# Kernel optimization log

Hardware: AMD Instinct MI355X
Metric: run time of the kernel (lower is better)

## Reference

```python
import jax, jax.numpy as jnp
import numpy as np

B, S, D = 32, 1024, 1024
A = 256           # adapter_size
E = 16            # num_domains
LN_EPS = 1e-5


def setup_inputs() -> dict:
    key = jax.random.key(0)
    ks = jax.random.split(key, 10)
    s = lambda fan_in: 1.0 / np.sqrt(fan_in)
    return {
        'hidden_states': jax.random.normal(ks[0], (B, S, D), dtype=jnp.float32),
        'domain_id': jax.random.randint(ks[1], (B,), 0, E, dtype=jnp.int64),
        'down_W': jax.random.uniform(ks[2], (A, D), jnp.float32, -s(D), s(D)),
        'down_b': jax.random.uniform(ks[3], (A,), jnp.float32, -s(D), s(D)),
        'up_W': jax.random.uniform(ks[4], (D, A), jnp.float32, -s(A), s(A)),
        'up_b': jax.random.uniform(ks[5], (D,), jnp.float32, -s(A), s(A)),
        'expert_W': jax.random.uniform(ks[6], (E, A, A), jnp.float32, -s(A), s(A)),
        'expert_b': jax.random.uniform(ks[7], (E, A), jnp.float32, -s(A), s(A)),
        'domain_emb': jax.random.normal(ks[8], (E, A), dtype=jnp.float32),
        'ln_gamma': jnp.ones((D,), jnp.float32),
        'ln_beta': jnp.zeros((D,), jnp.float32),
    }


def reference(hidden_states, domain_id, down_W, down_b, up_W, up_b,
              expert_W, expert_b, domain_emb, ln_gamma, ln_beta):
    residual = hidden_states
    # down projection + exact GELU (torch nn.GELU default)
    hidden = jnp.einsum('bsd,ad->bsa', hidden_states, down_W) + down_b
    hidden = jax.nn.gelu(hidden, approximate=False)
    # per-sample expert linear: gather each sample's expert weight, batched GEMM
    valid = (domain_id >= 0) & (domain_id < E)
    idx = jnp.clip(domain_id, 0, E - 1)
    Wsel = expert_W[idx]                      # [B, A, A]
    bsel = expert_b[idx]                      # [B, A]
    expert_out = jnp.einsum('bsa,boa->bso', hidden, Wsel) + bsel[:, None, :]
    domain_output = jnp.where(valid[:, None, None], expert_out, hidden)
    # add domain embedding broadcast over seq
    hidden = domain_output + domain_emb[idx][:, None, :]
    # up projection (dropout is identity at inference)
    hidden = jnp.einsum('bsa,da->bsd', hidden, up_W) + up_b
    # layer norm over last dim
    x = hidden + residual
    mu = jnp.mean(x, axis=-1, keepdims=True)
    var = jnp.mean(jnp.square(x - mu), axis=-1, keepdims=True)
    return (x - mu) * jax.lax.rsqrt(var + LN_EPS) * ln_gamma + ln_beta
```

## Files before the change

kernel.cpp:

```cpp
#include <hip/hip_runtime.h>
#include <hip/hip_bf16.h>
#include <math.h>

#define D_DIM 1024
#define A_DIM 256
#define E_NUM 16

typedef __attribute__((ext_vector_type(8))) short short8;
typedef __attribute__((ext_vector_type(4))) float f32x4;

__device__ __forceinline__ short f2bs(float x) {
    __hip_bfloat16 h = __float2bfloat16(x);
    return __builtin_bit_cast(short, h);
}
__device__ __forceinline__ float bs2f(short s) {
    __hip_bfloat16 h = __builtin_bit_cast(__hip_bfloat16, s);
    return __bfloat162float(h);
}
__device__ __forceinline__ float gelu_exact(float x) {
    return 0.5f * x * (1.0f + erff(x * 0.70710678118654752f));
}
__device__ __forceinline__ void gload_lds16(const void* g, void* l) {
    __builtin_amdgcn_global_load_lds(
        (const __attribute__((address_space(1))) void*)g,
        (__attribute__((address_space(3))) void*)l, 16, 0, 0);
}
__device__ __forceinline__ short8 pack8(float4 u, float4 v) {
    short8 pk;
    pk[0] = f2bs(u.x); pk[1] = f2bs(u.y); pk[2] = f2bs(u.z); pk[3] = f2bs(u.w);
    pk[4] = f2bs(v.x); pk[5] = f2bs(v.y); pk[6] = f2bs(v.z); pk[7] = f2bs(v.w);
    return pk;
}

__global__ __launch_bounds__(256) void k_cast_w(
    const float* __restrict__ Wd, const float* __restrict__ Wu,
    const float* __restrict__ eW,
    short* __restrict__ WdB, short* __restrict__ WuB, short* __restrict__ eWB)
{
    unsigned i = blockIdx.x * 256 + threadIdx.x;
    if (i < 131072) {
        const float4* s = (const float4*)eW;
        ((short8*)eWB)[i] = pack8(s[2 * (size_t)i], s[2 * (size_t)i + 1]);
    } else if (i < 163840) {
        unsigned j = i - 131072;
        const float4* s = (const float4*)Wd;
        ((short8*)WdB)[j] = pack8(s[2 * (size_t)j], s[2 * (size_t)j + 1]);
    } else {
        unsigned j = i - 163840;
        const float4* s = (const float4*)Wu;
        ((short8*)WuB)[j] = pack8(s[2 * (size_t)j], s[2 * (size_t)j + 1]);
    }
}

__global__ __launch_bounds__(256, 2) void k_down_expert(
    const float* __restrict__ X, const short* __restrict__ WdB,
    const float* __restrict__ bd, const short* __restrict__ eWB,
    const float* __restrict__ eb, const float* __restrict__ emb,
    const int* __restrict__ domain_id, short* __restrict__ H2)
{
    __shared__ short As[64][72];
    __shared__ short Bs[256][64];
    __shared__ short Hs[64][264];
    const int tid  = threadIdx.x;
    const int lane = tid & 63;
    const int w    = tid >> 6;
    const int quad = lane >> 4, cid = lane & 15;
    const int m0 = blockIdx.x * 64;

    const int samp = m0 >> 10;
    const int id = domain_id[samp];
    const bool valid = (id >= 0) && (id < E_NUM);
    const int idc = id < 0 ? 0 : (id > E_NUM - 1 ? E_NUM - 1 : id);

    f32x4 acc[4][4];
    #pragma unroll
    for (int i = 0; i < 4; i++)
        #pragma unroll
        for (int j = 0; j < 4; j++) acc[i][j] = (f32x4)(0.f);

    for (int kt = 0; kt < D_DIM; kt += 64) {
        #pragma unroll
        for (int p = 0; p < 8; p++) {
            int jj = tid + p * 256;
            int r = jj >> 3;
            int cg = (((jj & 7) ^ (r & 7)) * 8);
            int cl = (jj & 7) * 8;
            gload_lds16(WdB + (size_t)r * D_DIM + kt + cg, &Bs[r][cl]);
        }
        #pragma unroll
        for (int p = 0; p < 2; p++) {
            int jj = tid + p * 256;
            int r = jj >> 3, c = (jj & 7) * 8;
            const float4* src = (const float4*)(X + (size_t)(m0 + r) * D_DIM + kt + c);
            *(short8*)&As[r][c] = pack8(src[0], src[1]);
        }
        __syncthreads();
        #pragma unroll
        for (int kk = 0; kk < 2; kk++) {
            short8 a[4], b[4];
            #pragma unroll
            for (int i = 0; i < 4; i++)
                a[i] = *(const short8*)&As[i * 16 + cid][kk * 32 + quad * 8];
            #pragma unroll
            for (int j = 0; j < 4; j++)
                b[j] = *(const short8*)&Bs[w * 64 + j * 16 + cid]
                                         [(kk * 32 + quad * 8) ^ ((cid & 7) * 8)];
            #pragma unroll
            for (int i = 0; i < 4; i++)
                #pragma unroll
                for (int j = 0; j < 4; j++)
                    acc[i][j] = __builtin_amdgcn_mfma_f32_16x16x32_bf16(
                        a[i], b[j], acc[i][j], 0, 0, 0);
        }
        __syncthreads();
    }

    #pragma unroll
    for (int j = 0; j < 4; j++) {
        int col = w * 64 + j * 16 + cid;
        float bdv = bd[col];
        #pragma unroll
        for (int i = 0; i < 4; i++)
            #pragma unroll
            for (int r = 0; r < 4; r++)
                Hs[i * 16 + quad * 4 + r][col] = f2bs(gelu_exact(acc[i][j][r] + bdv));
    }

    f32x4 acc2[4][4];
    #pragma unroll
    for (int i = 0; i < 4; i++)
        #pragma unroll
        for (int j = 0; j < 4; j++) acc2[i][j] = (f32x4)(0.f);

    const short* Bsrc = eWB + (size_t)idc * A_DIM * A_DIM;
    for (int kt = 0; kt < A_DIM; kt += 64) {
        #pragma unroll
        for (int p = 0; p < 8; p++) {
            int jj = tid + p * 256;
            int r = jj >> 3;
            int cg = (((jj & 7) ^ (r & 7)) * 8);
            int cl = (jj & 7) * 8;
            gload_lds16(Bsrc + (size_t)r * A_DIM + kt + cg, &Bs[r][cl]);
        }
        __syncthreads();
        #pragma unroll
        for (int kk = 0; kk < 2; kk++) {
            short8 a[4], b[4];
            #pragma unroll
            for (int i = 0; i < 4; i++)
                a[i] = *(const short8*)&Hs[i * 16 + cid][kt + kk * 32 + quad * 8];
            #pragma unroll
            for (int j = 0; j < 4; j++)
                b[j] = *(const short8*)&Bs[w * 64 + j * 16 + cid]
                                         [(kk * 32 + quad * 8) ^ ((cid & 7) * 8)];
            #pragma unroll
            for (int i = 0; i < 4; i++)
                #pragma unroll
                for (int j = 0; j < 4; j++)
                    acc2[i][j] = __builtin_amdgcn_mfma_f32_16x16x32_bf16(
                        a[i], b[j], acc2[i][j], 0, 0, 0);
        }
        __syncthreads();
    }

    #pragma unroll
    for (int j = 0; j < 4; j++) {
        int col = w * 64 + j * 16 + cid;
        float ebv = eb[idc * A_DIM + col];
        float ev  = emb[idc * A_DIM + col];
        #pragma unroll
        for (int i = 0; i < 4; i++)
            #pragma unroll
            for (int r = 0; r < 4; r++) {
                int rl = i * 16 + quad * 4 + r;
                float base;
                if (valid) base = acc2[i][j][r] + ebv;
                else       base = bs2f(Hs[rl][col]);
                H2[(size_t)(m0 + rl) * A_DIM + col] = f2bs(base + ev);
            }
    }
}

__global__ __launch_bounds__(1024, 4) void k_up_ln(
    const short* __restrict__ H2, const short* __restrict__ WuB,
    const float* __restrict__ ub, const float* __restrict__ X,
    const float* __restrict__ gamma, const float* __restrict__ beta,
    float* __restrict__ out)
{
    __shared__ short As[32][264];
    __shared__ float redS[16][32], red2[16][32];
    __shared__ float muS[32], rsS[32];
    const int tid  = threadIdx.x;
    const int lane = tid & 63;
    const int w    = tid >> 6;
    const int quad = lane >> 4, cid = lane & 15;
    const int m0 = blockIdx.x * 32;
    const int nb = w * 64;

    const int pr = tid >> 5, pc = (tid & 31) * 8;
    short8 pv = *(const short8*)(H2 + (size_t)(m0 + pr) * A_DIM + pc);

    float xres[4][2][4];
    #pragma unroll
    for (int j = 0; j < 4; j++) {
        int col = nb + j * 16 + cid;
        #pragma unroll
        for (int mf = 0; mf < 2; mf++)
            #pragma unroll
            for (int r = 0; r < 4; r++)
                xres[j][mf][r] =
                    X[(size_t)(m0 + mf * 16 + quad * 4 + r) * D_DIM + col];
    }

    *(short8*)&As[pr][pc] = pv;
    __syncthreads();

    f32x4 acc[2][4];
    #pragma unroll
    for (int mf = 0; mf < 2; mf++)
        #pragma unroll
        for (int j = 0; j < 4; j++) acc[mf][j] = (f32x4)(0.f);

    const short* bbase = WuB + (size_t)(nb + cid) * A_DIM + quad * 8;

    #pragma unroll
    for (int kt = 0; kt < 4; kt++) {
        #pragma unroll
        for (int kk = 0; kk < 2; kk++) {
            short8 a0 = *(const short8*)&As[cid][kt * 64 + kk * 32 + quad * 8];
            short8 a1 = *(const short8*)&As[16 + cid][kt * 64 + kk * 32 + quad * 8];
            #pragma unroll
            for (int j = 0; j < 4; j++) {
                short8 b = *(const short8*)(bbase + (size_t)(j * 16) * A_DIM
                                            + kt * 64 + kk * 32);
                acc[0][j] = __builtin_amdgcn_mfma_f32_16x16x32_bf16(a0, b, acc[0][j], 0, 0, 0);
                acc[1][j] = __builtin_amdgcn_mfma_f32_16x16x32_bf16(a1, b, acc[1][j], 0, 0, 0);
            }
        }
    }

    float s1[2][4], s2[2][4];
    #pragma unroll
    for (int mf = 0; mf < 2; mf++)
        #pragma unroll
        for (int r = 0; r < 4; r++) { s1[mf][r] = 0.f; s2[mf][r] = 0.f; }
    #pragma unroll
    for (int j = 0; j < 4; j++) {
        int col = nb + j * 16 + cid;
        float ubv = ub[col];
        #pragma unroll
        for (int mf = 0; mf < 2; mf++)
            #pragma unroll
            for (int r = 0; r < 4; r++) {
                float x = acc[mf][j][r] + ubv + xres[j][mf][r];
                acc[mf][j][r] = x;
                s1[mf][r] += x;
                s2[mf][r] += x * x;
            }
    }
    #pragma unroll
    for (int mf = 0; mf < 2; mf++)
        #pragma unroll
        for (int r = 0; r < 4; r++) {
            float a = s1[mf][r], b = s2[mf][r];
            #pragma unroll
            for (int off = 1; off < 16; off <<= 1) {
                a += __shfl_xor(a, off, 64);
                b += __shfl_xor(b, off, 64);
            }
            if (cid == 0) {
                int rl = mf * 16 + quad * 4 + r;
                redS[w][rl] = a;
                red2[w][rl] = b;
            }
        }
    __syncthreads();
    if (tid < 32) {
        float S = 0.f, Q = 0.f;
        #pragma unroll
        for (int ww = 0; ww < 16; ww++) { S += redS[ww][tid]; Q += red2[ww][tid]; }
        float mu = S * (1.0f / 1024.0f);
        float var = Q * (1.0f / 1024.0f) - mu * mu;
        muS[tid] = mu;
        rsS[tid] = rsqrtf(var + 1e-5f);
    }
    __syncthreads();
    #pragma unroll
    for (int j = 0; j < 4; j++) {
        int col = nb + j * 16 + cid;
        float g = gamma[col], be = beta[col];
        #pragma unroll
        for (int mf = 0; mf < 2; mf++)
            #pragma unroll
            for (int r = 0; r < 4; r++) {
                int rl = mf * 16 + quad * 4 + r;
                out[(size_t)(m0 + rl) * D_DIM + col] =
                    (acc[mf][j][r] - muS[rl]) * rsS[rl] * g + be;
            }
    }
}

extern "C" void kernel_launch(void* const* d_in, const int* in_sizes, int n_in,
                              void* d_out, int out_size, void* d_ws, size_t ws_size,
                              hipStream_t stream) {
    const float* hs  = (const float*)d_in[0];
    const int*   did = (const int*)d_in[1];
    const float* dW  = (const float*)d_in[2];
    const float* db  = (const float*)d_in[3];
    const float* uW  = (const float*)d_in[4];
    const float* ub  = (const float*)d_in[5];
    const float* eW  = (const float*)d_in[6];
    const float* ebv = (const float*)d_in[7];
    const float* emb = (const float*)d_in[8];
    const float* gam = (const float*)d_in[9];
    const float* bet = (const float*)d_in[10];
    float* out = (float*)d_out;

    char* ws = (char*)d_ws;
    short* WdB = (short*)(ws);
    short* WuB = (short*)(ws + (1u << 19));
    short* eWB = (short*)(ws + (1u << 20));
    short* H2  = (short*)(ws + (3u << 20));

    k_cast_w     <<<768, 256, 0, stream>>>(dW, uW, eW, WdB, WuB, eWB);
    k_down_expert<<<512, 256, 0, stream>>>(hs, WdB, db, eWB, ebv, emb, did, H2);
    k_up_ln      <<<1024, 1024, 0, stream>>>(H2, WuB, ub, hs, gam, bet, out);
}
```

Measured before the change: 389.1 us.

## Prefetch next X tile in down GEMM; shrink up_ln blocks to 16 rows

In the down-projection kernel, the next K-tile of X is loaded into registers before the MFMA loop and written to LDS after the barrier, so global loads overlap with compute. The weight LDS load for the next tile is issued after compute as well. The up+LayerNorm kernel now uses 512-thread blocks, each covering 16 rows, with each wave producing 128 columns. It reads the residual inline rather than preloading it, which cuts per-block register and LDS use but doubles how often WuB is reloaded per row.

```diff
diff --git a/kernel.cpp b/kernel.cpp
--- a/kernel.cpp
+++ b/kernel.cpp
@@ -78,23 +78,34 @@
         #pragma unroll
         for (int j = 0; j < 4; j++) acc[i][j] = (f32x4)(0.f);
 
+    #pragma unroll
+    for (int p = 0; p < 8; p++) {
+        int jj = tid + p * 256;
+        int r = jj >> 3;
+        int cg = (((jj & 7) ^ (r & 7)) * 8);
+        int cl = (jj & 7) * 8;
+        gload_lds16(WdB + (size_t)r * D_DIM + cg, &Bs[r][cl]);
+    }
+    #pragma unroll
+    for (int p = 0; p < 2; p++) {
+        int jj = tid + p * 256;
+        int r = jj >> 3, c = (jj & 7) * 8;
+        const float4* src = (const float4*)(X + (size_t)(m0 + r) * D_DIM + c);
+        *(short8*)&As[r][c] = pack8(src[0], src[1]);
+    }
+    __syncthreads();
+
     for (int kt = 0; kt < D_DIM; kt += 64) {
-        #pragma unroll
-        for (int p = 0; p < 8; p++) {
-            int jj = tid + p * 256;
-            int r = jj >> 3;
-            int cg = (((jj & 7) ^ (r & 7)) * 8);
-            int cl = (jj & 7) * 8;
-            gload_lds16(WdB + (size_t)r * D_DIM + kt + cg, &Bs[r][cl]);
-        }
-        #pragma unroll
-        for (int p = 0; p < 2; p++) {
-            int jj = tid + p * 256;
-            int r = jj >> 3, c = (jj & 7) * 8;
-            const float4* src = (const float4*)(X + (size_t)(m0 + r) * D_DIM + kt + c);
-            *(short8*)&As[r][c] = pack8(src[0], src[1]);
-        }
-        __syncthreads();
+        const bool more = (kt + 64) < D_DIM;
+        float4 ap00, ap01, ap10, ap11;
+        if (more) {
+            int jj0 = tid, r0 = jj0 >> 3, c0 = (jj0 & 7) * 8;
+            const float4* s0 = (const float4*)(X + (size_t)(m0 + r0) * D_DIM + kt + 64 + c0);
+            ap00 = s0[0]; ap01 = s0[1];
+            int jj1 = tid + 256, r1 = jj1 >> 3, c1 = (jj1 & 7) * 8;
+            const float4* s1 = (const float4*)(X + (size_t)(m0 + r1) * D_DIM + kt + 64 + c1);
+            ap10 = s1[0]; ap11 = s1[1];
+        }
         #pragma unroll
         for (int kk = 0; kk < 2; kk++) {
             short8 a[4], b[4];
@@ -113,6 +124,23 @@
                         a[i], b[j], acc[i][j], 0, 0, 0);
         }
         __syncthreads();
+        if (more) {
+            #pragma unroll
+            for (int p = 0; p < 8; p++) {
+                int jj = tid + p * 256;
+                int r = jj >> 3;
+                int cg = (((jj & 7) ^ (r & 7)) * 8);
+                int cl = (jj & 7) * 8;
+                gload_lds16(WdB + (size_t)r * D_DIM + kt + 64 + cg, &Bs[r][cl]);
+            }
+            {
+                int jj0 = tid, r0 = jj0 >> 3, c0 = (jj0 & 7) * 8;
+                *(short8*)&As[r0][c0] = pack8(ap00, ap01);
+                int jj1 = tid + 256, r1 = jj1 >> 3, c1 = (jj1 & 7) * 8;
+                *(short8*)&As[r1][c1] = pack8(ap10, ap11);
+            }
+            __syncthreads();
+        }
     }
 
     #pragma unroll
@@ -181,45 +209,30 @@
     }
 }
 
-__global__ __launch_bounds__(1024, 4) void k_up_ln(
+__global__ __launch_bounds__(512, 4) void k_up_ln(
     const short* __restrict__ H2, const short* __restrict__ WuB,
     const float* __restrict__ ub, const float* __restrict__ X,
     const float* __restrict__ gamma, const float* __restrict__ beta,
     float* __restrict__ out)
 {
-    __shared__ short As[32][264];
-    __shared__ float redS[16][32], red2[16][32];
-    __shared__ float muS[32], rsS[32];
+    __shared__ short As[16][264];
+    __shared__ float redS[8][16], red2[8][16];
+    __shared__ float muS[16], rsS[16];
     const int tid  = threadIdx.x;
     const int lane = tid & 63;
     const int w    = tid >> 6;
     const int quad = lane >> 4, cid = lane & 15;
-    const int m0 = blockIdx.x * 32;
-    const int nb = w * 64;
+    const int m0 = blockIdx.x * 16;
+    const int nb = w * 128;
 
     const int pr = tid >> 5, pc = (tid & 31) * 8;
     short8 pv = *(const short8*)(H2 + (size_t)(m0 + pr) * A_DIM + pc);
-
-    float xres[4][2][4];
-    #pragma unroll
-    for (int j = 0; j < 4; j++) {
-        int col = nb + j * 16 + cid;
-        #pragma unroll
-        for (int mf = 0; mf < 2; mf++)
-            #pragma unroll
-            for (int r = 0; r < 4; r++)
-                xres[j][mf][r] =
-                    X[(size_t)(m0 + mf * 16 + quad * 4 + r) * D_DIM + col];
-    }
-
     *(short8*)&As[pr][pc] = pv;
     __syncthreads();
 
-    f32x4 acc[2][4];
-    #pragma unroll
-    for (int mf = 0; mf < 2; mf++)
-        #pragma unroll
-        for (int j = 0; j < 4; j++) acc[mf][j] = (f32x4)(0.f);
+    f32x4 acc[8];
+    #pragma unroll
+    for (int j = 0; j < 8; j++) acc[j] = (f32x4)(0.f);
 
     const short* bbase = WuB + (size_t)(nb + cid) * A_DIM + quad * 8;
 
@@ -228,57 +241,50 @@
         #pragma unroll
         for (int kk = 0; kk < 2; kk++) {
             short8 a0 = *(const short8*)&As[cid][kt * 64 + kk * 32 + quad * 8];
-            short8 a1 = *(const short8*)&As[16 + cid][kt * 64 + kk * 32 + quad * 8];
-            #pragma unroll
-            for (int j = 0; j < 4; j++) {
+            #pragma unroll
+            for (int j = 0; j < 8; j++) {
                 short8 b = *(const short8*)(bbase + (size_t)(j * 16) * A_DIM
                                             + kt * 64 + kk * 32);
-                acc[0][j] = __builtin_amdgcn_mfma_f32_16x16x32_bf16(a0, b, acc[0][j], 0, 0, 0);
-                acc[1][j] = __builtin_amdgcn_mfma_f32_16x16x32_bf16(a1, b, acc[1][j], 0, 0, 0);
+                acc[j] = __builtin_amdgcn_mfma_f32_16x16x32_bf16(a0, b, acc[j], 0, 0, 0);
             }
         }
     }
 
-    float s1[2][4], s2[2][4];
-    #pragma unroll
-    for (int mf = 0; mf < 2; mf++)
-        #pragma unroll
-        for (int r = 0; r < 4; r++) { s1[mf][r] = 0.f; s2[mf][r] = 0.f; }
-    #pragma unroll
-    for (int j = 0; j < 4; j++) {
+    float s1[4], s2[4];
+    #pragma unroll
+    for (int r = 0; r < 4; r++) { s1[r] = 0.f; s2[r] = 0.f; }
+    #pragma unroll
+    for (int j = 0; j < 8; j++) {
         int col = nb + j * 16 + cid;
         float ubv = ub[col];
         #pragma unroll
-        for (int mf = 0; mf < 2; mf++)
-            #pragma unroll
-            for (int r = 0; r < 4; r++) {
-                float x = acc[mf][j][r] + ubv + xres[j][mf][r];
-                acc[mf][j][r] = x;
-                s1[mf][r] += x;
-                s2[mf][r] += x * x;
-            }
-    }
-    #pragma unroll
-    for (int mf = 0; mf < 2; mf++)
-        #pragma unroll
         for (int r = 0; r < 4; r++) {
-            float a = s1[mf][r], b = s2[mf][r];
-            #pragma unroll
-            for (int off = 1; off < 16; off <<= 1) {
-                a += __shfl_xor(a, off, 64);
-                b += __shfl_xor(b, off, 64);
-            }
-            if (cid == 0) {
-                int rl = mf * 16 + quad * 4 + r;
-                redS[w][rl] = a;
-                red2[w][rl] = b;
-            }
-        }
+            int row = m0 + quad * 4 + r;
+            float x = acc[j][r] + ubv + X[(size_t)row * D_DIM + col];
+            acc[j][r] = x;
+            s1[r] += x;
+            s2[r] += x * x;
+        }
+    }
+    #pragma unroll
+    for (int r = 0; r < 4; r++) {
+        float a = s1[r], b = s2[r];
+        #pragma unroll
+        for (int off = 1; off < 16; off <<= 1) {
+            a += __shfl_xor(a, off, 64);
+            b += __shfl_xor(b, off, 64);
+        }
+        if (cid == 0) {
+            int rl = quad * 4 + r;
+            redS[w][rl] = a;
+            red2[w][rl] = b;
+        }
+    }
     __syncthreads();
-    if (tid < 32) {
+    if (tid < 16) {
         float S = 0.f, Q = 0.f;
         #pragma unroll
-        for (int ww = 0; ww < 16; ww++) { S += redS[ww][tid]; Q += red2[ww][tid]; }
+        for (int ww = 0; ww < 8; ww++) { S += redS[ww][tid]; Q += red2[ww][tid]; }
         float mu = S * (1.0f / 1024.0f);
         float var = Q * (1.0f / 1024.0f) - mu * mu;
         muS[tid] = mu;
@@ -286,17 +292,15 @@
     }
     __syncthreads();
     #pragma unroll
-    for (int j = 0; j < 4; j++) {
+    for (int j = 0; j < 8; j++) {
         int col = nb + j * 16 + cid;
         float g = gamma[col], be = beta[col];
         #pragma unroll
-        for (int mf = 0; mf < 2; mf++)
-            #pragma unroll
-            for (int r = 0; r < 4; r++) {
-                int rl = mf * 16 + quad * 4 + r;
-                out[(size_t)(m0 + rl) * D_DIM + col] =
-                    (acc[mf][j][r] - muS[rl]) * rsS[rl] * g + be;
-            }
+        for (int r = 0; r < 4; r++) {
+            int rl = quad * 4 + r;
+            out[(size_t)(m0 + rl) * D_DIM + col] =
+                (acc[j][r] - muS[rl]) * rsS[rl] * g + be;
+        }
     }
 }
 
@@ -324,5 +328,5 @@
 
     k_cast_w     <<<768, 256, 0, stream>>>(dW, uW, eW, WdB, WuB, eWB);
     k_down_expert<<<512, 256, 0, stream>>>(hs, WdB, db, eWB, ebv, emb, did, H2);
-    k_up_ln      <<<1024, 1024, 0, stream>>>(H2, WuB, ub, hs, gam, bet, out);
-}
+    k_up_ln      <<<2048, 512, 0, stream>>>(H2, WuB, ub, hs, gam, bet, out);
+}
```

Measured after the change: 396.1 us. About the same (+1.8%).

## Prefetch next K tile in down GEMM and pre-swizzle up weights for coalesced loads

Applied to the files above, without the earlier changes.

The down-projection loop now loads the first tile before the loop and issues global reads for the next X tile while MFMAs run on the current one. It then writes the next tile into LDS after a barrier, a single-buffer software pipeline. The up-projection weight is stored in an MFMA-fragment-ordered layout during the cast, so each wave reads contiguous 16-byte chunks and can register double-buffer the next K slice. The residual X loads move from the prologue into the LayerNorm epilogue, which lowers register pressure but exposes their latency later.

```diff
diff --git a/kernel.cpp b/kernel.cpp
--- a/kernel.cpp
+++ b/kernel.cpp
@@ -35,7 +35,7 @@
 __global__ __launch_bounds__(256) void k_cast_w(
     const float* __restrict__ Wd, const float* __restrict__ Wu,
     const float* __restrict__ eW,
-    short* __restrict__ WdB, short* __restrict__ WuB, short* __restrict__ eWB)
+    short* __restrict__ WdB, short* __restrict__ WuT, short* __restrict__ eWB)
 {
     unsigned i = blockIdx.x * 256 + threadIdx.x;
     if (i < 131072) {
@@ -48,7 +48,13 @@
     } else {
         unsigned j = i - 163840;
         const float4* s = (const float4*)Wu;
-        ((short8*)WuB)[j] = pack8(s[2 * (size_t)j], s[2 * (size_t)j + 1]);
+        short8 v = pack8(s[2 * (size_t)j], s[2 * (size_t)j + 1]);
+        unsigned d  = j >> 5;
+        unsigned k0 = (j & 31) * 8;
+        unsigned jg = d >> 4, cid = d & 15;
+        unsigned p  = k0 >> 5, quad = (k0 >> 3) & 3;
+        unsigned idx = ((jg * 8 + p) * 64 + quad * 16 + cid) * 8;
+        *(short8*)(WuT + idx) = v;
     }
 }
 
@@ -78,23 +84,34 @@
         #pragma unroll
         for (int j = 0; j < 4; j++) acc[i][j] = (f32x4)(0.f);
 
+    #pragma unroll
+    for (int p = 0; p < 8; p++) {
+        int jj = tid + p * 256;
+        int r = jj >> 3;
+        int cg = (((jj & 7) ^ (r & 7)) * 8);
+        int cl = (jj & 7) * 8;
+        gload_lds16(WdB + (size_t)r * D_DIM + cg, &Bs[r][cl]);
+    }
+    #pragma unroll
+    for (int p = 0; p < 2; p++) {
+        int jj = tid + p * 256;
+        int r = jj >> 3, c = (jj & 7) * 8;
+        const float4* src = (const float4*)(X + (size_t)(m0 + r) * D_DIM + c);
+        *(short8*)&As[r][c] = pack8(src[0], src[1]);
+    }
+    __syncthreads();
+
     for (int kt = 0; kt < D_DIM; kt += 64) {
-        #pragma unroll
-        for (int p = 0; p < 8; p++) {
-            int jj = tid + p * 256;
-            int r = jj >> 3;
-            int cg = (((jj & 7) ^ (r & 7)) * 8);
-            int cl = (jj & 7) * 8;
-            gload_lds16(WdB + (size_t)r * D_DIM + kt + cg, &Bs[r][cl]);
-        }
-        #pragma unroll
-        for (int p = 0; p < 2; p++) {
-            int jj = tid + p * 256;
-            int r = jj >> 3, c = (jj & 7) * 8;
-            const float4* src = (const float4*)(X + (size_t)(m0 + r) * D_DIM + kt + c);
-            *(short8*)&As[r][c] = pack8(src[0], src[1]);
-        }
-        __syncthreads();
+        const bool more = (kt + 64) < D_DIM;
+        float4 ap00, ap01, ap10, ap11;
+        if (more) {
+            int jj0 = tid, r0 = jj0 >> 3, c0 = (jj0 & 7) * 8;
+            const float4* s0 = (const float4*)(X + (size_t)(m0 + r0) * D_DIM + kt + 64 + c0);
+            ap00 = s0[0]; ap01 = s0[1];
+            int jj1 = tid + 256, r1 = jj1 >> 3, c1 = (jj1 & 7) * 8;
+            const float4* s1 = (const float4*)(X + (size_t)(m0 + r1) * D_DIM + kt + 64 + c1);
+            ap10 = s1[0]; ap11 = s1[1];
+        }
         #pragma unroll
         for (int kk = 0; kk < 2; kk++) {
             short8 a[4], b[4];
@@ -113,6 +130,23 @@
                         a[i], b[j], acc[i][j], 0, 0, 0);
         }
         __syncthreads();
+        if (more) {
+            #pragma unroll
+            for (int p = 0; p < 8; p++) {
+                int jj = tid + p * 256;
+                int r = jj >> 3;
+                int cg = (((jj & 7) ^ (r & 7)) * 8);
+                int cl = (jj & 7) * 8;
+                gload_lds16(WdB + (size_t)r * D_DIM + kt + 64 + cg, &Bs[r][cl]);
+            }
+            {
+                int jj0 = tid, r0 = jj0 >> 3, c0 = (jj0 & 7) * 8;
+                *(short8*)&As[r0][c0] = pack8(ap00, ap01);
+                int jj1 = tid + 256, r1 = jj1 >> 3, c1 = (jj1 & 7) * 8;
+                *(short8*)&As[r1][c1] = pack8(ap10, ap11);
+            }
+            __syncthreads();
+        }
     }
 
     #pragma unroll
@@ -182,7 +216,7 @@
 }
 
 __global__ __launch_bounds__(1024, 4) void k_up_ln(
-    const short* __restrict__ H2, const short* __restrict__ WuB,
+    const short* __restrict__ H2, const short* __restrict__ WuT,
     const float* __restrict__ ub, const float* __restrict__ X,
     const float* __restrict__ gamma, const float* __restrict__ beta,
     float* __restrict__ out)
@@ -199,19 +233,6 @@
 
     const int pr = tid >> 5, pc = (tid & 31) * 8;
     short8 pv = *(const short8*)(H2 + (size_t)(m0 + pr) * A_DIM + pc);
-
-    float xres[4][2][4];
-    #pragma unroll
-    for (int j = 0; j < 4; j++) {
-        int col = nb + j * 16 + cid;
-        #pragma unroll
-        for (int mf = 0; mf < 2; mf++)
-            #pragma unroll
-            for (int r = 0; r < 4; r++)
-                xres[j][mf][r] =
-                    X[(size_t)(m0 + mf * 16 + quad * 4 + r) * D_DIM + col];
-    }
-
     *(short8*)&As[pr][pc] = pv;
     __syncthreads();
 
@@ -221,21 +242,30 @@
         #pragma unroll
         for (int j = 0; j < 4; j++) acc[mf][j] = (f32x4)(0.f);
 
-    const short* bbase = WuB + (size_t)(nb + cid) * A_DIM + quad * 8;
-
-    #pragma unroll
-    for (int kt = 0; kt < 4; kt++) {
-        #pragma unroll
-        for (int kk = 0; kk < 2; kk++) {
-            short8 a0 = *(const short8*)&As[cid][kt * 64 + kk * 32 + quad * 8];
-            short8 a1 = *(const short8*)&As[16 + cid][kt * 64 + kk * 32 + quad * 8];
-            #pragma unroll
-            for (int j = 0; j < 4; j++) {
-                short8 b = *(const short8*)(bbase + (size_t)(j * 16) * A_DIM
-                                            + kt * 64 + kk * 32);
-                acc[0][j] = __builtin_amdgcn_mfma_f32_16x16x32_bf16(a0, b, acc[0][j], 0, 0, 0);
-                acc[1][j] = __builtin_amdgcn_mfma_f32_16x16x32_bf16(a1, b, acc[1][j], 0, 0, 0);
-            }
+    const short* bt = WuT + ((size_t)w * 32) * 512 + (size_t)lane * 8;
+
+    short8 bcur[4], bnxt[4];
+    #pragma unroll
+    for (int j = 0; j < 4; j++)
+        bcur[j] = *(const short8*)(bt + (size_t)(j * 8) * 512);
+
+    #pragma unroll
+    for (int p = 0; p < 8; p++) {
+        if (p < 7) {
+            #pragma unroll
+            for (int j = 0; j < 4; j++)
+                bnxt[j] = *(const short8*)(bt + (size_t)(j * 8 + p + 1) * 512);
+        }
+        short8 a0 = *(const short8*)&As[cid][p * 32 + quad * 8];
+        short8 a1 = *(const short8*)&As[16 + cid][p * 32 + quad * 8];
+        #pragma unroll
+        for (int j = 0; j < 4; j++) {
+            acc[0][j] = __builtin_amdgcn_mfma_f32_16x16x32_bf16(a0, bcur[j], acc[0][j], 0, 0, 0);
+            acc[1][j] = __builtin_amdgcn_mfma_f32_16x16x32_bf16(a1, bcur[j], acc[1][j], 0, 0, 0);
+        }
+        if (p < 7) {
+            #pragma unroll
+            for (int j = 0; j < 4; j++) bcur[j] = bnxt[j];
         }
     }
 
@@ -252,7 +282,8 @@
         for (int mf = 0; mf < 2; mf++)
             #pragma unroll
             for (int r = 0; r < 4; r++) {
-                float x = acc[mf][j][r] + ubv + xres[j][mf][r];
+                int row = m0 + mf * 16 + quad * 4 + r;
+                float x = acc[mf][j][r] + ubv + X[(size_t)row * D_DIM + col];
                 acc[mf][j][r] = x;
                 s1[mf][r] += x;
                 s2[mf][r] += x * x;
@@ -318,11 +349,11 @@
 
     char* ws = (char*)d_ws;
     short* WdB = (short*)(ws);
-    short* WuB = (short*)(ws + (1u << 19));
+    short* WuT = (short*)(ws + (1u << 19));
     short* eWB = (short*)(ws + (1u << 20));
     short* H2  = (short*)(ws + (3u << 20));
 
-    k_cast_w     <<<768, 256, 0, stream>>>(dW, uW, eW, WdB, WuB, eWB);
+    k_cast_w     <<<768, 256, 0, stream>>>(dW, uW, eW, WdB, WuT, eWB);
     k_down_expert<<<512, 256, 0, stream>>>(hs, WdB, db, eWB, ebv, emb, did, H2);
-    k_up_ln      <<<1024, 1024, 0, stream>>>(H2, WuB, ub, hs, gam, bet, out);
-}
+    k_up_ln      <<<1024, 1024, 0, stream>>>(H2, WuT, ub, hs, gam, bet, out);
+}
```

Result: faster. 337.3 us (-13.3%).
